# Performance work log

Measured on AMD Instinct MI355X. Metric: run time of the kernel, lower is better.

## Reference

```python
import jax, jax.numpy as jnp
import numpy as np

B, S, D = 32, 1, 2048
H, KVH, HD = 16, 4, 128
MAXS = 4096
EPS = 1e-5
NREP = H // KVH  # GQA repeat factor = 4
FF = 4 * D
POS = 4095  # decode position (start_pos)


def setup_inputs() -> dict:
    key = jax.random.key(0)
    ks = jax.random.split(key, 12)
    sc = lambda d: 1.0 / np.sqrt(d)
    # RoPE angles for the current token position, [S, HD//2]
    inv_freq = 1.0 / (10000.0 ** (np.arange(0, HD, 2, dtype=np.float32) / HD))
    ang = (POS + np.arange(S, dtype=np.float32))[:, None] * inv_freq[None, :]
    return {
        "x": jax.random.normal(ks[0], (B, S, D), jnp.float32),
        "cos": jnp.asarray(np.cos(ang), jnp.float32),
        "sin": jnp.asarray(np.sin(ang), jnp.float32),
        "k_cache": jax.random.normal(ks[1], (B, MAXS, KVH, HD), jnp.float32),
        "v_cache": jax.random.normal(ks[2], (B, MAXS, KVH, HD), jnp.float32),
        "w_rms_attn": jnp.ones((D,), jnp.float32),
        "wq": jax.random.normal(ks[3], (D, D), jnp.float32) * sc(D),
        "wk": jax.random.normal(ks[4], (D, KVH * HD), jnp.float32) * sc(D),
        "wv": jax.random.normal(ks[5], (D, KVH * HD), jnp.float32) * sc(D),
        "wo": jax.random.normal(ks[6], (D, D), jnp.float32) * sc(D),
        "w_rms_ffn": jnp.ones((D,), jnp.float32),
        "w1": jax.random.normal(ks[7], (D, FF), jnp.float32) * sc(D),
        "w2": jax.random.normal(ks[8], (D, FF), jnp.float32) * sc(D),
        "w3": jax.random.normal(ks[9], (FF, D), jnp.float32) * sc(FF),
        "start_pos": POS,
    }


def _rmsnorm(x, g):
    return x * g * jax.lax.rsqrt(jnp.mean(x * x, axis=-1, keepdims=True) + EPS)


def _rope(x, cos, sin):
    # x: [B, S, h, HD]; complex rotation on (even, odd) pairs
    xr = x.reshape(*x.shape[:-1], HD // 2, 2)
    x0, x1 = xr[..., 0], xr[..., 1]
    c = cos[None, :, None, :]
    s = sin[None, :, None, :]
    r0 = x0 * c - x1 * s
    r1 = x0 * s + x1 * c
    return jnp.stack([r0, r1], axis=-1).reshape(x.shape)


def reference(x, cos, sin, k_cache, v_cache, w_rms_attn, wq, wk, wv, wo,
              w_rms_ffn, w1, w2, w3, start_pos):
    xa = _rmsnorm(x, w_rms_attn)
    xq = (xa @ wq).reshape(B, S, H, HD)
    xk = (xa @ wk).reshape(B, S, KVH, HD)
    xv = (xa @ wv).reshape(B, S, KVH, HD)
    # Source applies RoPE to K and V (not Q) -- reproduced faithfully.
    xk = _rope(xk, cos, sin)
    xv = _rope(xv, cos, sin)
    kc = jax.lax.dynamic_update_slice(k_cache, xk, (0, start_pos, 0, 0))
    vc = jax.lax.dynamic_update_slice(v_cache, xv, (0, start_pos, 0, 0))
    klen = start_pos + S
    keys = jnp.repeat(kc[:, :klen], NREP, axis=2)   # [B, klen, H, HD]
    vals = jnp.repeat(vc[:, :klen], NREP, axis=2)
    att = jnp.einsum('bqhd,bkhd->bhqk', xq, keys) * (HD ** -0.5)
    att = jax.nn.softmax(att, axis=-1)
    y = jnp.einsum('bhqk,bkhd->bqhd', att, vals).reshape(B, S, D)
    h = x + y @ wo
    xf = _rmsnorm(h, w_rms_ffn)
    return h + (jax.nn.silu(xf @ w1) * (xf @ w2)) @ w3
```

## Files before the change

### kernel.cpp

```cpp
#include <hip/hip_runtime.h>
#include <math.h>

#define BB 32
#define DD 2048
#define NKVH 4
#define HDIM 128
#define MAXS 4096
#define FFD 8192
#define POS 4095
#define EPSV 1e-5f
#define SCALE 0.08838834764831845f
#define ASPLIT 32
#define SPOS 128

#define OFF_QT   0u
#define OFF_KT   65536u
#define OFF_VT   81920u
#define OFF_G1   98304u
#define OFF_G2   360448u
#define ZERO_N   622592u
#define OFF_XAT  622592u
#define OFF_RK   688128u
#define OFF_RV   704512u
#define OFF_PML  720896u
#define OFF_PACC 753664u
#define OFF_YT   2850816u
#define OFF_H    2916352u
#define OFF_XFT  2981888u
#define OFF_KFIX 3047424u
#define OFF_VFIX 3309568u

#define VM_WAIT8 asm volatile("s_waitcnt vmcnt(8)" ::: "memory")
#define VM_WAIT0 asm volatile("s_waitcnt vmcnt(0)" ::: "memory")
#define LG_WAIT0 asm volatile("s_waitcnt lgkmcnt(0)" ::: "memory")
#define SCHED0   __builtin_amdgcn_sched_barrier(0)
#define SBAR     __builtin_amdgcn_s_barrier()

#define REP32(M) M(0) M(1) M(2) M(3) M(4) M(5) M(6) M(7) M(8) M(9) M(10) M(11) M(12) M(13) M(14) M(15) M(16) M(17) M(18) M(19) M(20) M(21) M(22) M(23) M(24) M(25) M(26) M(27) M(28) M(29) M(30) M(31)
#define REP32A(M,X) M(0,X) M(1,X) M(2,X) M(3,X) M(4,X) M(5,X) M(6,X) M(7,X) M(8,X) M(9,X) M(10,X) M(11,X) M(12,X) M(13,X) M(14,X) M(15,X) M(16,X) M(17,X) M(18,X) M(19,X) M(20,X) M(21,X) M(22,X) M(23,X) M(24,X) M(25,X) M(26,X) M(27,X) M(28,X) M(29,X) M(30,X) M(31,X)

#define DECLA(i) float a##i = 0.f;
#define FMA1(i,k) a##i = fmaf(ap[(k)*32 + (i)], w##k, a##i);
#define STORET(i) tl[i] = a##i;
#define ATOMN(i) atomicAdd(C + (size_t)(i)*N + n, a##i);

template<int N, int CH, bool TOUT>
__device__ __forceinline__ void gemv_body(const float* __restrict__ At,
                                          const float* __restrict__ W,
                                          float* __restrict__ C, int colblk,
                                          float* tile) {
    int tid = (int)threadIdx.x;
    int n = colblk * 256 + tid;
    int d0 = blockIdx.y * CH;
    const float* Wp = W + (size_t)d0 * N + n;
    const float* ap = At + (size_t)d0 * 32;
    REP32(DECLA)
#pragma unroll 4
    for (int dd = 0; dd < CH; dd += 4) {
        float w0 = Wp[0];
        float w1 = Wp[(size_t)N];
        float w2 = Wp[(size_t)N * 2];
        float w3 = Wp[(size_t)N * 3];
        REP32A(FMA1, 0)
        REP32A(FMA1, 1)
        REP32A(FMA1, 2)
        REP32A(FMA1, 3)
        Wp += (size_t)N * 4;
        ap += 128;
    }
    if constexpr (TOUT) {
        float* tl = tile + tid * 33;
        REP32(STORET)
        __syncthreads();
        float* cb = C + (size_t)colblk * 256 * 32;
#pragma unroll
        for (int i = 0; i < 32; ++i) {
            int f = i * 256 + tid;
            atomicAdd(cb + f, tile[(f >> 5) * 33 + (f & 31)]);
        }
    } else {
        REP32(ATOMN)
    }
}

template<int N, int CH, bool TOUT>
__global__ __launch_bounds__(256) void gemv32_kernel(const float* __restrict__ At,
                                                     const float* __restrict__ W,
                                                     float* __restrict__ C) {
    if constexpr (TOUT) {
        __shared__ float tile[256 * 33];
        gemv_body<N, CH, true>(At, W, C, blockIdx.x, tile);
    } else {
        gemv_body<N, CH, false>(At, W, C, blockIdx.x, nullptr);
    }
}

template<int N, int CH, int HALF>
__global__ __launch_bounds__(256) void gemv32_dual_kernel(const float* __restrict__ At,
        const float* __restrict__ W0, const float* __restrict__ W1,
        float* __restrict__ C0, float* __restrict__ C1) {
    __shared__ float tile[256 * 33];
    int bx = blockIdx.x;
    if (bx < HALF) gemv_body<N, CH, true>(At, W0, C0, bx, tile);
    else           gemv_body<N, CH, true>(At, W1, C1, bx - HALF, tile);
}

__global__ void zero_kernel(float* __restrict__ p) {
    p[blockIdx.x * 256 + threadIdx.x] = 0.f;
}

__global__ void rmsnorm_kernel(const float* __restrict__ in, const float* __restrict__ g,
                               float* __restrict__ outT, float* __restrict__ cpy) {
    int b = blockIdx.x;
    int tid = threadIdx.x;
    const float* row = in + b * DD;
    float v[8];
    float ss = 0.f;
#pragma unroll
    for (int i = 0; i < 8; ++i) { v[i] = row[tid + i * 256]; ss += v[i] * v[i]; }
#pragma unroll
    for (int off = 32; off; off >>= 1) ss += __shfl_xor(ss, off);
    __shared__ float red[4];
    if ((tid & 63) == 0) red[tid >> 6] = ss;
    __syncthreads();
    ss = red[0] + red[1] + red[2] + red[3];
    float scale = rsqrtf(ss * (1.f / DD) + EPSV);
#pragma unroll
    for (int i = 0; i < 8; ++i) {
        int idx = tid + i * 256;
        outT[(size_t)idx * 32 + b] = v[i] * g[idx] * scale;
        if (cpy) cpy[b * DD + idx] = v[i];
    }
}

__global__ void rope_kernel(const float* __restrict__ kT, const float* __restrict__ vT,
                            const float* __restrict__ cosb, const float* __restrict__ sinb,
                            float* __restrict__ rk, float* __restrict__ rv) {
    int idx = blockIdx.x * 256 + threadIdx.x;
    int b = idx >> 8, rem = idx & 255;
    int kvh = rem >> 6, i = rem & 63;
    float c = cosb[i], s = sinb[i];
    int col = kvh * HDIM + 2 * i;
    float k0 = kT[(size_t)col * 32 + b], k1 = kT[(size_t)(col + 1) * 32 + b];
    float v0 = vT[(size_t)col * 32 + b], v1 = vT[(size_t)(col + 1) * 32 + b];
    int o = (b * NKVH + kvh) * HDIM + 2 * i;
    rk[o] = k0 * c - k1 * s; rk[o + 1] = k0 * s + k1 * c;
    rv[o] = v0 * c - v1 * s; rv[o + 1] = v0 * s + v1 * c;
}

__global__ void fixlast_kernel(const float* __restrict__ kc, const float* __restrict__ vc,
                               const float* __restrict__ rk, const float* __restrict__ rv,
                               float* __restrict__ kfix, float* __restrict__ vfix) {
    int idx = blockIdx.x * 256 + threadIdx.x;
    int b = idx >> 13, rem = idx & 8191;
    int pos = rem >> 9, col = rem & 511;
    int gpos = 4080 + pos;
    float kv, vv;
    if (gpos == POS) {
        kv = rk[b * 512 + col]; vv = rv[b * 512 + col];
    } else {
        size_t o = ((size_t)(b * MAXS + gpos)) * 512 + col;
        kv = kc[o]; vv = vc[o];
    }
    kfix[idx] = kv; vfix[idx] = vv;
}

__global__ __launch_bounds__(256, 2) void attn_stage_kernel(
    const float* __restrict__ qn, const float* __restrict__ kc, const float* __restrict__ vc,
    const float* __restrict__ kfix, const float* __restrict__ vfix,
    float* __restrict__ pml, float* __restrict__ pacc) {
    int split = blockIdx.x & 31, b = blockIdx.x >> 5;
    int tid = threadIdx.x, lane = tid & 63, wv = tid >> 6;
    __shared__ float kbuf[2][8192];
    __shared__ float p_s[128][16];
    int qpos = tid >> 4, qhead = tid & 15;
    int qr = qpos * 4 + (qhead >> 2);
    int vh = tid >> 4, c16 = tid & 15, vkvh = vh >> 2;
    int t0 = split * SPOS;

    float4 qrot[32];
#pragma unroll
    for (int j = 0; j < 32; ++j) {
        int g = (j + qr) & 31;
        qrot[j] = *(const float4*)(qn + (size_t)b * DD + qhead * HDIM + g * 4);
    }
    float4 av0 = {0, 0, 0, 0}, av1 = {0, 0, 0, 0};

    auto stage = [&](int t) {
        int s = t & 7;
        const float* base;
        if (t < 8) base = (split == 31 && s == 7) ? kfix + (size_t)b * 8192
                                                  : kc + ((size_t)b * MAXS + t0 + s * 16) * 512;
        else       base = (split == 31 && s == 7) ? vfix + (size_t)b * 8192
                                                  : vc + ((size_t)b * MAXS + t0 + s * 16) * 512;
        const float* g = base + wv * 2048 + lane * 4;
        float* l = &kbuf[t & 1][wv * 2048];
#pragma unroll
        for (int i = 0; i < 8; ++i)
            __builtin_amdgcn_global_load_lds(
                (const __attribute__((address_space(1))) void*)(g + i * 256),
                (__attribute__((address_space(3))) void*)(l + i * 256), 16, 0, 0);
    };

    stage(0);
    for (int t = 0; t < 16; ++t) {
        if (t < 15) { stage(t + 1); VM_WAIT8; } else { VM_WAIT0; }
        SCHED0; SBAR;
        if (t == 8) {
#pragma unroll
            for (int hh = 0; hh < 4; ++hh) {
                int h = wv * 4 + hh;
                float e0 = p_s[lane][h], e1 = p_s[lane + 64][h];
                float m = fmaxf(e0, e1);
#pragma unroll
                for (int off = 32; off; off >>= 1) m = fmaxf(m, __shfl_xor(m, off));
                e0 = __expf(e0 - m); e1 = __expf(e1 - m);
                p_s[lane][h] = e0; p_s[lane + 64][h] = e1;
                float l2 = e0 + e1;
#pragma unroll
                for (int off = 32; off; off >>= 1) l2 += __shfl_xor(l2, off);
                if (lane == 0) {
                    int idx = ((b * ASPLIT + split) * 16 + h) * 2;
                    pml[idx] = m; pml[idx + 1] = l2;
                }
            }
        }
        const float* kb = kbuf[t & 1];
        if (t < 8) {
            float4 acc = {0, 0, 0, 0};
            const float* rowp = kb + qr * 128;
#pragma unroll
            for (int j = 0; j < 32; ++j) {
                int g = (j + qr) & 31;
                float4 k4 = *(const float4*)(rowp + g * 4);
                acc.x = fmaf(k4.x, qrot[j].x, acc.x);
                acc.y = fmaf(k4.y, qrot[j].y, acc.y);
                acc.z = fmaf(k4.z, qrot[j].z, acc.z);
                acc.w = fmaf(k4.w, qrot[j].w, acc.w);
            }
            p_s[t * 16 + qpos][qhead] = (acc.x + acc.y + acc.z + acc.w) * SCALE;
        } else {
            int s = t - 8;
            const float* vrow = kb + vkvh * 128 + c16 * 4;
#pragma unroll
            for (int p = 0; p < 16; ++p) {
                float pw = p_s[s * 16 + p][vh];
                float4 v0 = *(const float4*)(vrow + p * 512);
                float4 v1 = *(const float4*)(vrow + p * 512 + 64);
                av0.x = fmaf(pw, v0.x, av0.x); av0.y = fmaf(pw, v0.y, av0.y);
                av0.z = fmaf(pw, v0.z, av0.z); av0.w = fmaf(pw, v0.w, av0.w);
                av1.x = fmaf(pw, v1.x, av1.x); av1.y = fmaf(pw, v1.y, av1.y);
                av1.z = fmaf(pw, v1.z, av1.z); av1.w = fmaf(pw, v1.w, av1.w);
            }
        }
        LG_WAIT0; SCHED0; SBAR;
    }
    size_t pbase = ((size_t)(b * ASPLIT + split) * 16 + vh) * HDIM;
    *(float4*)(pacc + pbase + c16 * 4) = av0;
    *(float4*)(pacc + pbase + 64 + c16 * 4) = av1;
}

__global__ void attn_combine_kernel(const float* __restrict__ pml,
                                    const float* __restrict__ pacc, float* __restrict__ yT) {
    int bid = blockIdx.x;
    int b = bid >> 4, h = bid & 15;
    int d = threadIdx.x;
    float M = -INFINITY;
#pragma unroll 8
    for (int s = 0; s < ASPLIT; ++s)
        M = fmaxf(M, pml[((b * ASPLIT + s) * 16 + h) * 2]);
    float denom = 0.f, acc = 0.f;
#pragma unroll 4
    for (int s = 0; s < ASPLIT; ++s) {
        int idx = (b * ASPLIT + s) * 16 + h;
        float e = __expf(pml[idx * 2] - M);
        denom += pml[idx * 2 + 1] * e;
        acc += e * pacc[(size_t)idx * HDIM + d];
    }
    yT[(size_t)(h * HDIM + d) * 32 + b] = acc / denom;
}

__global__ void silu_mul_kernel(float* __restrict__ g1, const float* __restrict__ g2) {
    int i = blockIdx.x * 256 + threadIdx.x;
    float a = g1[i], bb = g2[i];
    g1[i] = a * bb / (1.f + __expf(-a));
}

extern "C" void kernel_launch(void* const* d_in, const int* in_sizes, int n_in,
                              void* d_out, int out_size, void* d_ws, size_t ws_size,
                              hipStream_t stream) {
    (void)in_sizes; (void)n_in; (void)out_size; (void)ws_size;
    const float* x    = (const float*)d_in[0];
    const float* cosb = (const float*)d_in[1];
    const float* sinb = (const float*)d_in[2];
    const float* kc   = (const float*)d_in[3];
    const float* vc   = (const float*)d_in[4];
    const float* wra  = (const float*)d_in[5];
    const float* wq   = (const float*)d_in[6];
    const float* wk   = (const float*)d_in[7];
    const float* wv   = (const float*)d_in[8];
    const float* wo   = (const float*)d_in[9];
    const float* wrf  = (const float*)d_in[10];
    const float* w1   = (const float*)d_in[11];
    const float* w2   = (const float*)d_in[12];
    const float* w3   = (const float*)d_in[13];
    float* out = (float*)d_out;
    float* ws  = (float*)d_ws;

    float* qn   = ws + OFF_QT;
    float* kT   = ws + OFF_KT;
    float* vT   = ws + OFF_VT;
    float* g1T  = ws + OFF_G1;
    float* g2T  = ws + OFF_G2;
    float* xaT  = ws + OFF_XAT;
    float* rk   = ws + OFF_RK;
    float* rv   = ws + OFF_RV;
    float* pml  = ws + OFF_PML;
    float* pacc = ws + OFF_PACC;
    float* yT   = ws + OFF_YT;
    float* h    = ws + OFF_H;
    float* xfT  = ws + OFF_XFT;
    float* kfix = ws + OFF_KFIX;
    float* vfix = ws + OFF_VFIX;

    zero_kernel<<<ZERO_N / 256, 256, 0, stream>>>(ws);

    rmsnorm_kernel<<<32, 256, 0, stream>>>(x, wra, xaT, h);
    gemv32_kernel<2048, 32, false><<<dim3(8, 64), 256, 0, stream>>>(xaT, wq, qn);
    gemv32_dual_kernel<512, 32, 2><<<dim3(4, 64), 256, 0, stream>>>(xaT, wk, wv, kT, vT);
    rope_kernel<<<32, 256, 0, stream>>>(kT, vT, cosb, sinb, rk, rv);
    fixlast_kernel<<<1024, 256, 0, stream>>>(kc, vc, rk, rv, kfix, vfix);
    attn_stage_kernel<<<1024, 256, 0, stream>>>(qn, kc, vc, kfix, vfix, pml, pacc);
    attn_combine_kernel<<<512, 128, 0, stream>>>(pml, pacc, yT);
    gemv32_kernel<2048, 32, false><<<dim3(8, 64), 256, 0, stream>>>(yT, wo, h);
    rmsnorm_kernel<<<32, 256, 0, stream>>>(h, wrf, xfT, out);
    gemv32_dual_kernel<8192, 128, 32><<<dim3(64, 16), 256, 0, stream>>>(xfT, w1, w2, g1T, g2T);
    silu_mul_kernel<<<1024, 256, 0, stream>>>(g1T, g2T);
    gemv32_kernel<2048, 128, false><<<dim3(8, 64), 256, 0, stream>>>(g1T, w3, out);
}
```

Before: 309.7 us.

## Triple-buffer attention K/V staging, fuse RoPE into fixup, widen GEMV columns

The attention stage kernel now keeps three LDS buffers and issues loads two stages ahead, waiting on vmcnt(16). It drops the per-iteration lgkmcnt wait and lowers the occupancy hint to one block per CU. The separate RoPE kernel is folded into the last-position fixup kernel, removing one launch and its intermediate buffers. The non-transposed GEMVs now process two columns per thread with float2 loads over half as many blocks, aiming for wider memory accesses in exchange for more registers and fewer waves.

```diff
diff --git a/kernel.cpp b/kernel.cpp
--- a/kernel.cpp
+++ b/kernel.cpp
@@ -20,8 +20,6 @@
 #define OFF_G2   360448u
 #define ZERO_N   622592u
 #define OFF_XAT  622592u
-#define OFF_RK   688128u
-#define OFF_RV   704512u
 #define OFF_PML  720896u
 #define OFF_PACC 753664u
 #define OFF_YT   2850816u
@@ -30,11 +28,11 @@
 #define OFF_KFIX 3047424u
 #define OFF_VFIX 3309568u
 
-#define VM_WAIT8 asm volatile("s_waitcnt vmcnt(8)" ::: "memory")
-#define VM_WAIT0 asm volatile("s_waitcnt vmcnt(0)" ::: "memory")
-#define LG_WAIT0 asm volatile("s_waitcnt lgkmcnt(0)" ::: "memory")
-#define SCHED0   __builtin_amdgcn_sched_barrier(0)
-#define SBAR     __builtin_amdgcn_s_barrier()
+#define VM_WAIT16 asm volatile("s_waitcnt vmcnt(16)" ::: "memory")
+#define VM_WAIT8  asm volatile("s_waitcnt vmcnt(8)" ::: "memory")
+#define VM_WAIT0  asm volatile("s_waitcnt vmcnt(0)" ::: "memory")
+#define SCHED0    __builtin_amdgcn_sched_barrier(0)
+#define SBAR      __builtin_amdgcn_s_barrier()
 
 #define REP32(M) M(0) M(1) M(2) M(3) M(4) M(5) M(6) M(7) M(8) M(9) M(10) M(11) M(12) M(13) M(14) M(15) M(16) M(17) M(18) M(19) M(20) M(21) M(22) M(23) M(24) M(25) M(26) M(27) M(28) M(29) M(30) M(31)
 #define REP32A(M,X) M(0,X) M(1,X) M(2,X) M(3,X) M(4,X) M(5,X) M(6,X) M(7,X) M(8,X) M(9,X) M(10,X) M(11,X) M(12,X) M(13,X) M(14,X) M(15,X) M(16,X) M(17,X) M(18,X) M(19,X) M(20,X) M(21,X) M(22,X) M(23,X) M(24,X) M(25,X) M(26,X) M(27,X) M(28,X) M(29,X) M(30,X) M(31,X)
@@ -42,13 +40,12 @@
 #define DECLA(i) float a##i = 0.f;
 #define FMA1(i,k) a##i = fmaf(ap[(k)*32 + (i)], w##k, a##i);
 #define STORET(i) tl[i] = a##i;
-#define ATOMN(i) atomicAdd(C + (size_t)(i)*N + n, a##i);
-
-template<int N, int CH, bool TOUT>
-__device__ __forceinline__ void gemv_body(const float* __restrict__ At,
-                                          const float* __restrict__ W,
-                                          float* __restrict__ C, int colblk,
-                                          float* tile) {
+
+template<int N, int CH>
+__device__ __forceinline__ void gemv_body_t(const float* __restrict__ At,
+                                            const float* __restrict__ W,
+                                            float* __restrict__ C, int colblk,
+                                            float* tile) {
     int tid = (int)threadIdx.x;
     int n = colblk * 256 + tid;
     int d0 = blockIdx.y * CH;
@@ -68,30 +65,14 @@
         Wp += (size_t)N * 4;
         ap += 128;
     }
-    if constexpr (TOUT) {
-        float* tl = tile + tid * 33;
-        REP32(STORET)
-        __syncthreads();
-        float* cb = C + (size_t)colblk * 256 * 32;
-#pragma unroll
-        for (int i = 0; i < 32; ++i) {
-            int f = i * 256 + tid;
-            atomicAdd(cb + f, tile[(f >> 5) * 33 + (f & 31)]);
-        }
-    } else {
-        REP32(ATOMN)
-    }
-}
-
-template<int N, int CH, bool TOUT>
-__global__ __launch_bounds__(256) void gemv32_kernel(const float* __restrict__ At,
-                                                     const float* __restrict__ W,
-                                                     float* __restrict__ C) {
-    if constexpr (TOUT) {
-        __shared__ float tile[256 * 33];
-        gemv_body<N, CH, true>(At, W, C, blockIdx.x, tile);
-    } else {
-        gemv_body<N, CH, false>(At, W, C, blockIdx.x, nullptr);
+    float* tl = tile + tid * 33;
+    REP32(STORET)
+    __syncthreads();
+    float* cb = C + (size_t)colblk * 256 * 32;
+#pragma unroll
+    for (int i = 0; i < 32; ++i) {
+        int f = i * 256 + tid;
+        atomicAdd(cb + f, tile[(f >> 5) * 33 + (f & 31)]);
     }
 }
 
@@ -101,8 +82,41 @@
         float* __restrict__ C0, float* __restrict__ C1) {
     __shared__ float tile[256 * 33];
     int bx = blockIdx.x;
-    if (bx < HALF) gemv_body<N, CH, true>(At, W0, C0, bx, tile);
-    else           gemv_body<N, CH, true>(At, W1, C1, bx - HALF, tile);
+    if (bx < HALF) gemv_body_t<N, CH>(At, W0, C0, bx, tile);
+    else           gemv_body_t<N, CH>(At, W1, C1, bx - HALF, tile);
+}
+
+#define DECL2(i) float2 a##i = {0.f, 0.f};
+#define FMA2(i,k) { float av = ap[(k)*32 + (i)]; \
+    a##i.x = fmaf(av, w##k.x, a##i.x); a##i.y = fmaf(av, w##k.y, a##i.y); }
+#define ATOM2(i) atomicAdd(Cb + (size_t)(i)*N, a##i.x); \
+                 atomicAdd(Cb + (size_t)(i)*N + 1, a##i.y);
+
+template<int N, int CH>
+__global__ __launch_bounds__(256) void gemv2_kernel(const float* __restrict__ At,
+                                                    const float* __restrict__ W,
+                                                    float* __restrict__ C) {
+    int tid = (int)threadIdx.x;
+    int n = blockIdx.x * 512 + tid * 2;
+    int d0 = blockIdx.y * CH;
+    const float* Wp = W + (size_t)d0 * N + n;
+    const float* ap = At + (size_t)d0 * 32;
+    REP32(DECL2)
+#pragma unroll 4
+    for (int dd = 0; dd < CH; dd += 4) {
+        float2 w0 = *(const float2*)(Wp);
+        float2 w1 = *(const float2*)(Wp + (size_t)N);
+        float2 w2 = *(const float2*)(Wp + (size_t)N * 2);
+        float2 w3 = *(const float2*)(Wp + (size_t)N * 3);
+        REP32A(FMA2, 0)
+        REP32A(FMA2, 1)
+        REP32A(FMA2, 2)
+        REP32A(FMA2, 3)
+        Wp += (size_t)N * 4;
+        ap += 128;
+    }
+    float* Cb = C + n;
+    REP32(ATOM2)
 }
 
 __global__ void zero_kernel(float* __restrict__ p) {
@@ -133,23 +147,9 @@
     }
 }
 
-__global__ void rope_kernel(const float* __restrict__ kT, const float* __restrict__ vT,
-                            const float* __restrict__ cosb, const float* __restrict__ sinb,
-                            float* __restrict__ rk, float* __restrict__ rv) {
-    int idx = blockIdx.x * 256 + threadIdx.x;
-    int b = idx >> 8, rem = idx & 255;
-    int kvh = rem >> 6, i = rem & 63;
-    float c = cosb[i], s = sinb[i];
-    int col = kvh * HDIM + 2 * i;
-    float k0 = kT[(size_t)col * 32 + b], k1 = kT[(size_t)(col + 1) * 32 + b];
-    float v0 = vT[(size_t)col * 32 + b], v1 = vT[(size_t)(col + 1) * 32 + b];
-    int o = (b * NKVH + kvh) * HDIM + 2 * i;
-    rk[o] = k0 * c - k1 * s; rk[o + 1] = k0 * s + k1 * c;
-    rv[o] = v0 * c - v1 * s; rv[o + 1] = v0 * s + v1 * c;
-}
-
-__global__ void fixlast_kernel(const float* __restrict__ kc, const float* __restrict__ vc,
-                               const float* __restrict__ rk, const float* __restrict__ rv,
+__global__ void fixrope_kernel(const float* __restrict__ kc, const float* __restrict__ vc,
+                               const float* __restrict__ kT, const float* __restrict__ vT,
+                               const float* __restrict__ cosb, const float* __restrict__ sinb,
                                float* __restrict__ kfix, float* __restrict__ vfix) {
     int idx = blockIdx.x * 256 + threadIdx.x;
     int b = idx >> 13, rem = idx & 8191;
@@ -157,7 +157,13 @@
     int gpos = 4080 + pos;
     float kv, vv;
     if (gpos == POS) {
-        kv = rk[b * 512 + col]; vv = rv[b * 512 + col];
+        int d = col & 127, i = d >> 1;
+        float c = cosb[i], s = sinb[i];
+        int colp = col & ~1;
+        float k0 = kT[(size_t)colp * 32 + b], k1 = kT[(size_t)(colp + 1) * 32 + b];
+        float v0 = vT[(size_t)colp * 32 + b], v1 = vT[(size_t)(colp + 1) * 32 + b];
+        if (d & 1) { kv = k0 * s + k1 * c; vv = v0 * s + v1 * c; }
+        else       { kv = k0 * c - k1 * s; vv = v0 * c - v1 * s; }
     } else {
         size_t o = ((size_t)(b * MAXS + gpos)) * 512 + col;
         kv = kc[o]; vv = vc[o];
@@ -165,13 +171,13 @@
     kfix[idx] = kv; vfix[idx] = vv;
 }
 
-__global__ __launch_bounds__(256, 2) void attn_stage_kernel(
+__global__ __launch_bounds__(256, 1) void attn_stage_kernel(
     const float* __restrict__ qn, const float* __restrict__ kc, const float* __restrict__ vc,
     const float* __restrict__ kfix, const float* __restrict__ vfix,
     float* __restrict__ pml, float* __restrict__ pacc) {
     int split = blockIdx.x & 31, b = blockIdx.x >> 5;
     int tid = threadIdx.x, lane = tid & 63, wv = tid >> 6;
-    __shared__ float kbuf[2][8192];
+    __shared__ float kbuf[3][8192];
     __shared__ float p_s[128][16];
     int qpos = tid >> 4, qhead = tid & 15;
     int qr = qpos * 4 + (qhead >> 2);
@@ -194,7 +200,7 @@
         else       base = (split == 31 && s == 7) ? vfix + (size_t)b * 8192
                                                   : vc + ((size_t)b * MAXS + t0 + s * 16) * 512;
         const float* g = base + wv * 2048 + lane * 4;
-        float* l = &kbuf[t & 1][wv * 2048];
+        float* l = &kbuf[t % 3][wv * 2048];
 #pragma unroll
         for (int i = 0; i < 8; ++i)
             __builtin_amdgcn_global_load_lds(
@@ -202,9 +208,11 @@
                 (__attribute__((address_space(3))) void*)(l + i * 256), 16, 0, 0);
     };
 
-    stage(0);
+    stage(0); stage(1);
     for (int t = 0; t < 16; ++t) {
-        if (t < 15) { stage(t + 1); VM_WAIT8; } else { VM_WAIT0; }
+        if (t < 14) { stage(t + 2); VM_WAIT16; }
+        else if (t == 14) { VM_WAIT8; }
+        else { VM_WAIT0; }
         SCHED0; SBAR;
         if (t == 8) {
 #pragma unroll
@@ -225,7 +233,7 @@
                 }
             }
         }
-        const float* kb = kbuf[t & 1];
+        const float* kb = kbuf[t % 3];
         if (t < 8) {
             float4 acc = {0, 0, 0, 0};
             const float* rowp = kb + qr * 128;
@@ -253,7 +261,7 @@
                 av1.z = fmaf(pw, v1.z, av1.z); av1.w = fmaf(pw, v1.w, av1.w);
             }
         }
-        LG_WAIT0; SCHED0; SBAR;
+        SCHED0; SBAR;
     }
     size_t pbase = ((size_t)(b * ASPLIT + split) * 16 + vh) * HDIM;
     *(float4*)(pacc + pbase + c16 * 4) = av0;
@@ -313,8 +321,6 @@
     float* g1T  = ws + OFF_G1;
     float* g2T  = ws + OFF_G2;
     float* xaT  = ws + OFF_XAT;
-    float* rk   = ws + OFF_RK;
-    float* rv   = ws + OFF_RV;
     float* pml  = ws + OFF_PML;
     float* pacc = ws + OFF_PACC;
     float* yT   = ws + OFF_YT;
@@ -326,15 +332,14 @@
     zero_kernel<<<ZERO_N / 256, 256, 0, stream>>>(ws);
 
     rmsnorm_kernel<<<32, 256, 0, stream>>>(x, wra, xaT, h);
-    gemv32_kernel<2048, 32, false><<<dim3(8, 64), 256, 0, stream>>>(xaT, wq, qn);
+    gemv2_kernel<2048, 32><<<dim3(4, 64), 256, 0, stream>>>(xaT, wq, qn);
     gemv32_dual_kernel<512, 32, 2><<<dim3(4, 64), 256, 0, stream>>>(xaT, wk, wv, kT, vT);
-    rope_kernel<<<32, 256, 0, stream>>>(kT, vT, cosb, sinb, rk, rv);
-    fixlast_kernel<<<1024, 256, 0, stream>>>(kc, vc, rk, rv, kfix, vfix);
+    fixrope_kernel<<<1024, 256, 0, stream>>>(kc, vc, kT, vT, cosb, sinb, kfix, vfix);
     attn_stage_kernel<<<1024, 256, 0, stream>>>(qn, kc, vc, kfix, vfix, pml, pacc);
     attn_combine_kernel<<<512, 128, 0, stream>>>(pml, pacc, yT);
-    gemv32_kernel<2048, 32, false><<<dim3(8, 64), 256, 0, stream>>>(yT, wo, h);
+    gemv2_kernel<2048, 32><<<dim3(4, 64), 256, 0, stream>>>(yT, wo, h);
     rmsnorm_kernel<<<32, 256, 0, stream>>>(h, wrf, xfT, out);
     gemv32_dual_kernel<8192, 128, 32><<<dim3(64, 16), 256, 0, stream>>>(xfT, w1, w2, g1T, g2T);
     silu_mul_kernel<<<1024, 256, 0, stream>>>(g1T, g2T);
-    gemv32_kernel<2048, 128, false><<<dim3(8, 64), 256, 0, stream>>>(g1T, w3, out);
-}
+    gemv2_kernel<2048, 128><<<dim3(4, 64), 256, 0, stream>>>(g1T, w3, out);
+}
```

New measurement: 396.9 us. +28.1%, slower.
